# Kernel tuning notes

Hardware: AMD Instinct MI355X
Metric: run time of the kernel (lower is better)

Reference implementation:

```python
import jax, jax.numpy as jnp
import numpy as np
import math

B, S, D, H = 4, 1024, 1024, 16
DK = D // H
K_INDEX = 5


def setup_inputs() -> dict:
    key = jax.random.key(0)
    ks = jax.random.split(key, 10)
    s = 0.02
    return {
        "query": jax.random.normal(ks[0], (B, S, D), jnp.float32),
        "key": jax.random.normal(ks[1], (B, S, D), jnp.float32),
        "values": jax.random.normal(ks[2], (B, S, D), jnp.float32),
        "lens": jax.random.randint(ks[3], (B,), 0, S),
        "Wq": jax.random.normal(ks[4], (D, D), jnp.float32) * s,  # shared q/k proj (kq_same=True)
        "bq": jnp.zeros((D,), jnp.float32),
        "Wv": jax.random.normal(ks[5], (D, D), jnp.float32) * s,
        "bv": jnp.zeros((D,), jnp.float32),
        "Wo": jax.random.normal(ks[6], (D, D), jnp.float32) * s,
        "bo": jnp.zeros((D,), jnp.float32),
        "gammas": jax.random.normal(ks[7], (H, 1, 1), jnp.float32) * 0.1,
        "ln_w": jnp.ones((D,), jnp.float32),
        "ln_b": jnp.zeros((D,), jnp.float32),
    }


def _split_heads(x):
    b, s, _ = x.shape
    return x.reshape(b, s, H, DK).transpose(0, 2, 1, 3)  # [B,H,S,DK]


def reference(query, key, values, lens, Wq, bq, Wv, bv, Wo, bo, gammas, ln_w, ln_b):
    # causal mask, peek_cur=False -> strict lower triangle; eval mode (no random masking)
    mask = jnp.tril(jnp.ones((S, S), bool), -1)[None, None]  # [1,1,S,S]

    q = _split_heads(query @ Wq.T + bq)
    k = _split_heads(key @ Wq.T + bq)   # kq_same: shared weights
    v = _split_heads(values @ Wv.T + bv)

    scores = jnp.einsum("bhid,bhjd->bhij", q, k) / math.sqrt(DK)
    NEG = jnp.finfo(scores.dtype).min

    # --- distance-decay term (no_grad in torch -> stop_gradient) ---
    s_ = jax.nn.softmax(jnp.where(mask, scores, NEG), axis=-1)
    distcum = jnp.cumsum(s_, axis=-1)
    disttotal = jnp.sum(s_, axis=-1, keepdims=True)
    idx = jnp.arange(S, dtype=scores.dtype)
    pos_effect = jnp.abs(idx[None, :] - idx[:, None])[None, None]  # |j - i|
    dist = jnp.sqrt(jnp.clip((disttotal - distcum) * pos_effect, 0.0, None))
    dist = jax.lax.stop_gradient(dist)

    gam = -jnp.abs(gammas)[None]  # [1,H,1,1]
    total_effect = jnp.clip(jnp.exp(dist * gam), 1e-5, 1e5)
    scores = scores * total_effect

    scores = jnp.where(mask, scores, NEG)
    p = jax.nn.softmax(scores, axis=-1)
    p = jnp.where(mask, p, 0.0)

    # maxout rescale (peek_cur=False)
    scale = jnp.minimum(1.0 / jnp.max(p, axis=-1, keepdims=True), 5.0)
    p = p * scale

    attn = jnp.einsum("bhij,bhjd->bhid", p, v)
    concat = attn.transpose(0, 2, 1, 3).reshape(B, S, D)
    attn_out = concat @ Wo.T + bo

    # k_select sparsification of the (post-softmax, maxout-scaled) scores
    sc_a = p[:, :, :K_INDEX, :]
    sc_b = p[:, :, K_INDEX:, :]
    kth = jax.lax.top_k(sc_b, K_INDEX)[0][..., -1:]  # k-th largest per row
    sc_b = jnp.where(sc_b >= kth, sc_b, NEG)
    sparse_scores = jax.nn.softmax(jnp.concatenate([sc_a, sc_b], axis=2), axis=-1)

    # residual (eval: dropout is identity) + LayerNorm
    y = query + attn_out
    mu = jnp.mean(y, axis=-1, keepdims=True)
    var = jnp.mean((y - mu) ** 2, axis=-1, keepdims=True)
    out = (y - mu) / jnp.sqrt(var + 1e-5) * ln_w + ln_b
    return (out, sparse_scores)
```

## Files before the change

### kernel.cpp

```cpp
#include <hip/hip_runtime.h>
#include <hip/hip_fp16.h>

#define Ssz 1024
#define Dsz 1024
#define Hsz 16
#define DKsz 64
#define Bsz 4
#define NEGI (-1.0e30f)
#define NEGD (-1.0e300)

typedef float f32x4 __attribute__((ext_vector_type(4)));
typedef _Float16 f16x8 __attribute__((ext_vector_type(8)));
typedef _Float16 f16x4 __attribute__((ext_vector_type(4)));

__device__ __forceinline__ float wmaxf(float x) {
#pragma unroll
  for (int o = 32; o; o >>= 1) x = fmaxf(x, __shfl_xor(x, o));
  return x;
}
__device__ __forceinline__ float wsumf(float x) {
#pragma unroll
  for (int o = 32; o; o >>= 1) x += __shfl_xor(x, o);
  return x;
}
__device__ __forceinline__ double wmaxd(double x) {
#pragma unroll
  for (int o = 32; o; o >>= 1) x = fmax(x, __shfl_xor(x, o));
  return x;
}
__device__ __forceinline__ double wsumd(double x) {
#pragma unroll
  for (int o = 32; o; o >>= 1) x += __shfl_xor(x, o);
  return x;
}
__device__ __forceinline__ int wmini(int x) {
#pragma unroll
  for (int o = 32; o; o >>= 1) x = min(x, __shfl_xor(x, o));
  return x;
}
__device__ __forceinline__ int sswz(int c) { return c ^ (((c >> 5) & 7) << 2); }
__device__ __forceinline__ int pswz(int c, int r) { return c ^ (r & 7) ^ ((c >> 3) & 7); }

__global__ __launch_bounds__(256) void wsplit_qv(
    const float* __restrict__ Wq, const float* __restrict__ Wv,
    __half* __restrict__ wqhi, __half* __restrict__ wqlo, __half* __restrict__ wvhi) {
  const size_t i = ((size_t)blockIdx.x * 256 + threadIdx.x) * 4;
  const f32x4 q = *(const f32x4*)(Wq + i);
  const f32x4 v = *(const f32x4*)(Wv + i);
  f16x4 hq, lq, hv;
#pragma unroll
  for (int e = 0; e < 4; e++) {
    const _Float16 h = (_Float16)q[e];
    hq[e] = h;
    lq[e] = (_Float16)(q[e] - (float)h);
    hv[e] = (_Float16)v[e];
  }
  *(f16x4*)((_Float16*)wqhi + i) = hq;
  *(f16x4*)((_Float16*)wqlo + i) = lq;
  *(f16x4*)((_Float16*)wvhi + i) = hv;
}

__global__ __launch_bounds__(256) void wsplit_o(
    const float* __restrict__ Wo, __half* __restrict__ wohi) {
  const size_t i = ((size_t)blockIdx.x * 256 + threadIdx.x) * 4;
  const f32x4 v = *(const f32x4*)(Wo + i);
  f16x4 hv;
#pragma unroll
  for (int e = 0; e < 4; e++) hv[e] = (_Float16)v[e];
  *(f16x4*)((_Float16*)wohi + i) = hv;
}

__global__ __launch_bounds__(256) void gemm_qk(
    const float* __restrict__ A, const __half* __restrict__ wqhi,
    const __half* __restrict__ wqlo, const float* __restrict__ bias,
    __half* __restrict__ ohi, __half* __restrict__ olo) {
  const int w = threadIdx.x >> 6, lane = threadIdx.x & 63;
  const int quad = lane >> 4, l16 = lane & 15;
  const int m0 = blockIdx.x * 64 + w * 16;
  const int n0 = blockIdx.y * 64;
  f32x4 acc[4] = {};
  const size_t arow = (size_t)(m0 + l16) * Dsz;
  for (int k0 = 0; k0 < Dsz; k0 += 32) {
    f16x8 ahi, alo;
    {
      const float* ap = A + arow + k0 + quad * 8;
#pragma unroll
      for (int e = 0; e < 8; e++) {
        const float v = ap[e];
        const _Float16 h = (_Float16)v;
        ahi[e] = h;
        alo[e] = (_Float16)(v - (float)h);
      }
    }
#pragma unroll
    for (int t = 0; t < 4; t++) {
      const size_t woff = (size_t)(n0 + t * 16 + l16) * Dsz + k0 + quad * 8;
      const f16x8 whi = *(const f16x8*)((const _Float16*)wqhi + woff);
      const f16x8 wlo = *(const f16x8*)((const _Float16*)wqlo + woff);
      acc[t] = __builtin_amdgcn_mfma_f32_16x16x32_f16(ahi, whi, acc[t], 0, 0, 0);
      acc[t] = __builtin_amdgcn_mfma_f32_16x16x32_f16(ahi, wlo, acc[t], 0, 0, 0);
      acc[t] = __builtin_amdgcn_mfma_f32_16x16x32_f16(alo, whi, acc[t], 0, 0, 0);
    }
  }
#pragma unroll
  for (int t = 0; t < 4; t++) {
    const int oc = n0 + t * 16 + l16;
    const float bv = bias[oc];
    const int hh = oc >> 6, dk = oc & 63;
#pragma unroll
    for (int r = 0; r < 4; r++) {
      const int mr = m0 + quad * 4 + r;
      const int bb = mr >> 10, ss = mr & 1023;
      const float v = acc[t][r] + bv;
      const size_t idx = ((size_t)(bb * Hsz + hh) * Ssz + ss) * DKsz + dk;
      const __half h = __float2half(v);
      ohi[idx] = h;
      olo[idx] = __float2half(v - __half2float(h));
    }
  }
}

__global__ __launch_bounds__(256) void gemm_v(
    const float* __restrict__ A, const __half* __restrict__ wvhi,
    const float* __restrict__ bias, __half* __restrict__ out_t) {
  const int w = threadIdx.x >> 6, lane = threadIdx.x & 63;
  const int quad = lane >> 4, l16 = lane & 15;
  const int m0 = blockIdx.x * 64 + w * 16;
  const int n0 = blockIdx.y * 64;
  f32x4 acc[4] = {};
  const size_t arow = (size_t)(m0 + l16) * Dsz;
  for (int k0 = 0; k0 < Dsz; k0 += 32) {
    f16x8 ahi;
    {
      const float* ap = A + arow + k0 + quad * 8;
#pragma unroll
      for (int e = 0; e < 8; e++) ahi[e] = (_Float16)ap[e];
    }
#pragma unroll
    for (int t = 0; t < 4; t++) {
      const size_t woff = (size_t)(n0 + t * 16 + l16) * Dsz + k0 + quad * 8;
      const f16x8 whi = *(const f16x8*)((const _Float16*)wvhi + woff);
      acc[t] = __builtin_amdgcn_mfma_f32_16x16x32_f16(ahi, whi, acc[t], 0, 0, 0);
    }
  }
#pragma unroll
  for (int t = 0; t < 4; t++) {
    const int oc = n0 + t * 16 + l16;
    const float bv = bias[oc];
    const int hh = oc >> 6, dk = oc & 63;
#pragma unroll
    for (int r = 0; r < 4; r++) {
      const int mr = m0 + quad * 4 + r;
      const int bb = mr >> 10, ss = mr & 1023;
      out_t[((size_t)(bb * Hsz + hh) * DKsz + dk) * Ssz + ss] = __float2half(acc[t][r] + bv);
    }
  }
}

__global__ __launch_bounds__(256) void gemm_o(
    const __half* __restrict__ A, const __half* __restrict__ wohi,
    const float* __restrict__ bias, float* __restrict__ outf) {
  const int w = threadIdx.x >> 6, lane = threadIdx.x & 63;
  const int quad = lane >> 4, l16 = lane & 15;
  const int m0 = blockIdx.x * 64 + w * 16;
  const int n0 = blockIdx.y * 64;
  f32x4 acc[4] = {};
  const size_t arow = (size_t)(m0 + l16) * Dsz;
  for (int k0 = 0; k0 < Dsz; k0 += 32) {
    const f16x8 a = *(const f16x8*)(A + arow + k0 + quad * 8);
#pragma unroll
    for (int t = 0; t < 4; t++) {
      const size_t woff = (size_t)(n0 + t * 16 + l16) * Dsz + k0 + quad * 8;
      const f16x8 whi = *(const f16x8*)((const _Float16*)wohi + woff);
      acc[t] = __builtin_amdgcn_mfma_f32_16x16x32_f16(a, whi, acc[t], 0, 0, 0);
    }
  }
#pragma unroll
  for (int t = 0; t < 4; t++) {
    const int oc = n0 + t * 16 + l16;
    const float bv = bias[oc];
#pragma unroll
    for (int r = 0; r < 4; r++) {
      const int mr = m0 + quad * 4 + r;
      outf[(size_t)mr * Dsz + oc] = acc[t][r] + bv;
    }
  }
}


__global__ __launch_bounds__(256) void attn_scores(
    const __half* __restrict__ qhi, const __half* __restrict__ qlo,
    const __half* __restrict__ khi, const __half* __restrict__ klo,
    float* __restrict__ scores, int bh0) {
  const int w = threadIdx.x >> 6, lane = threadIdx.x & 63;
  const int quad = lane >> 4, l16 = lane & 15;
  const int lbh = blockIdx.y, bh = bh0 + lbh;
  for (int cc = 0; cc < 2; cc++) {
    const int chunk = cc ? (63 - (int)blockIdx.x) : (int)blockIdx.x;
    const int i0 = chunk * 16;
    const size_t qb = ((size_t)bh * Ssz + i0 + l16) * DKsz + quad * 8;
    const f16x8 ah0 = *(const f16x8*)(qhi + qb);
    const f16x8 ah1 = *(const f16x8*)(qhi + qb + 32);
    const f16x8 al0 = *(const f16x8*)(qlo + qb);
    const f16x8 al1 = *(const f16x8*)(qlo + qb + 32);
    float* dst = scores + ((size_t)lbh * Ssz + i0) * Ssz;
    for (int tt = 0; tt < 16; tt++) {
      const int n0 = (w + tt * 4) * 16;
      if (n0 > i0 + 14) continue;
      const size_t kb = ((size_t)bh * Ssz + n0 + l16) * DKsz + quad * 8;
      const f16x8 bh0v = *(const f16x8*)(khi + kb);
      const f16x8 bh1v = *(const f16x8*)(khi + kb + 32);
      const f16x8 bl0v = *(const f16x8*)(klo + kb);
      const f16x8 bl1v = *(const f16x8*)(klo + kb + 32);
      f32x4 accs = {};
      accs = __builtin_amdgcn_mfma_f32_16x16x32_f16(al0, bl0v, accs, 0, 0, 0);
      accs = __builtin_amdgcn_mfma_f32_16x16x32_f16(al1, bl1v, accs, 0, 0, 0);
      accs = __builtin_amdgcn_mfma_f32_16x16x32_f16(ah0, bl0v, accs, 0, 0, 0);
      accs = __builtin_amdgcn_mfma_f32_16x16x32_f16(ah1, bl1v, accs, 0, 0, 0);
      accs = __builtin_amdgcn_mfma_f32_16x16x32_f16(al0, bh0v, accs, 0, 0, 0);
      accs = __builtin_amdgcn_mfma_f32_16x16x32_f16(al1, bh1v, accs, 0, 0, 0);
      accs = __builtin_amdgcn_mfma_f32_16x16x32_f16(ah0, bh0v, accs, 0, 0, 0);
      accs = __builtin_amdgcn_mfma_f32_16x16x32_f16(ah1, bh1v, accs, 0, 0, 0);
#pragma unroll
      for (int r = 0; r < 4; r++)
        dst[(size_t)(quad * 4 + r) * Ssz + n0 + l16] = accs[r] * 0.125f;
    }
  }
}

__global__ __launch_bounds__(256) void attn_soft(
    float* __restrict__ scores, const float* __restrict__ gam,
    float* __restrict__ sparse, int bh0) {
  const int w = threadIdx.x >> 6, lane = threadIdx.x & 63;
  const int lbh = blockIdx.y, bh = bh0 + lbh;
  const int hidx = bh & 15;
  const float gf = -fabsf(gam[hidx]);
  for (int cc = 0; cc < 2; cc++) {
    const int chunk = cc ? (63 - (int)blockIdx.x) : (int)blockIdx.x;
    const int i0 = chunk * 16;
    for (int rr = 0; rr < 4; rr++) {
      const int gi = i0 + w * 4 + rr;
      const int nch = __builtin_amdgcn_readfirstlane((gi + 63) >> 6);
      float* rowp = scores + ((size_t)lbh * Ssz + gi) * Ssz;
      float xf[16];
      float m1 = NEGI;
#pragma unroll
      for (int e = 0; e < 16; e++) {
        if (e < nch) {
          const int j = 64 * e + lane;
          xf[e] = rowp[j];
          if (j < gi) m1 = fmaxf(m1, xf[e]);
        }
      }
      m1 = wmaxf(m1);
      float s[16];
      float ls = 0.f;
#pragma unroll
      for (int e = 0; e < 16; e++) {
        s[e] = 0.f;
        if (e < nch) {
          const int j = 64 * e + lane;
          const float v = (j < gi) ? __expf(xf[e] - m1) : 0.f;
          s[e] = v;
          ls += v;
        }
      }
      ls = wsumf(ls);
      const float invls = (ls > 0.f) ? 1.0f / ls : 0.f;
      float tot[16];
#pragma unroll
      for (int e = 0; e < 16; e++) {
        if (e < nch) {
          const float q = s[e] * invls;
          float v = __shfl_down(q, 1);
          if (lane == 63) v = 0.f;
#pragma unroll
          for (int o = 1; o < 64; o <<= 1) {
            const float t = __shfl_down(v, o);
            if (lane + o < 64) v += t;
          }
          s[e] = v;
          tot[e] = __shfl(q + v, 0);
        }
      }
      {
        float csum = 0.f;
#pragma unroll
        for (int e = 15; e >= 0; e--) {
          if (e < nch) {
            s[e] = s[e] + csum;
            csum += tot[e];
          }
        }
      }
      float ys[16];
      float m2 = NEGI;
#pragma unroll
      for (int e = 0; e < 16; e++) {
        ys[e] = NEGI;
        if (e < nch) {
          const int j = 64 * e + lane;
          if (j < gi) {
            const float pe = (float)(gi - j);
            const float tl = s[e] > 0.f ? s[e] * pe : 0.f;
            float te = __expf(gf * sqrtf(tl));
            te = te < 1e-5f ? 1e-5f : te;
            const float vv = xf[e] * te;
            ys[e] = vv;
            m2 = fmaxf(m2, vv);
          }
        }
      }
      m2 = wmaxf(m2);
      float xs[16];
      float ls3 = 0.f, mev = 0.f;
#pragma unroll
      for (int e = 0; e < 16; e++) {
        xs[e] = 0.f;
        if (e < nch) {
          const int j = 64 * e + lane;
          const float ev = (j < gi) ? __expf(ys[e] - m2) : 0.f;
          xs[e] = ev;
          ls3 += ev;
          mev = fmaxf(mev, ev);
        }
      }
      ls3 = wsumf(ls3);
      mev = wmaxf(mev);
      const float inv2 = (ls3 > 0.f) ? 1.0f / ls3 : 0.f;
      const float mp = mev * inv2;
      const float scl = (mp > 0.f) ? fminf(1.0f / mp, 5.0f) : 5.0f;
      const float c2 = inv2 * scl;
#pragma unroll
      for (int e = 0; e < 16; e++) xs[e] *= c2;
      const float m3 = mp * scl;
      {
        _Float16* prow = (_Float16*)rowp;
#pragma unroll
        for (int e = 0; e < 16; e++) prow[64 * e + lane] = (_Float16)xs[e];
      }

      float* dst = sparse + ((size_t)bh * Ssz + gi) * Ssz;
      if (gi < 5) {
        float o4[16];
        float ls4 = 0.f;
#pragma unroll
        for (int e = 0; e < 16; e++) {
          const float ev = expf(xs[e] - m3);
          o4[e] = ev;
          ls4 += ev;
        }
        const float inv3 = 1.0f / fmaxf(wsumf(ls4), 1e-30f);
#pragma unroll
        for (int e = 0; e < 16; e++) dst[64 * e + lane] = o4[e] * inv3;
      } else {
        float m5 = 0.f, m6 = 0.f;
        {
          unsigned int removed = 0;
          for (int r6 = 0; r6 < 6; r6++) {
            float lm = NEGI;
#pragma unroll
            for (int e = 0; e < 16; e++)
              if (!((removed >> e) & 1)) lm = fmaxf(lm, ys[e]);
            const float m = wmaxf(lm);
            const unsigned long long bal = __ballot(lm == m);
            const int src = __ffsll(bal) - 1;
            int rem_e = 0;
#pragma unroll
            for (int e = 15; e >= 0; e--)
              if (!((removed >> e) & 1) && ys[e] == m) rem_e = e;
            if (lane == src) removed |= 1u << rem_e;
            if (r6 == 4) m5 = m;
            if (r6 == 5) m6 = m;
          }
        }
        const float bstar = 0.5f * (m5 + m6);
        const float ETA = 6e-5f;
        const float wlo = m6 - 0.1f, whi = m5 + 0.1f;
        float md[16];
        float mn = 0.f;
#pragma unroll
        for (int e = 0; e < 16; e++) {
          md[e] = 0.f;
          if (e < nch) {
            const int j = 64 * e + lane;
            if (j < gi && ys[e] >= wlo && ys[e] <= whi) {
              const float pe = (float)(gi - j);
              const float t0 = fmaxf(s[e], 0.f);
              float telo = __expf(gf * sqrtf(fmaxf(t0 - ETA, 0.f) * pe));
              telo = fminf(fmaxf(telo, 1e-5f), 1.0f);
              float tehi = __expf(gf * sqrtf((t0 + ETA) * pe));
              tehi = fminf(fmaxf(tehi, 1e-5f), 1.0f);
              md[e] = fminf(fabsf(xf[e]) * (telo - tehi) + 2e-4f, 0.04f);
              mn = fmaxf(mn, md[e]);
            }
          }
        }
        mn = wmaxf(mn);
        float cnt = 0.f;
        unsigned int mK = 0, mA = 0;
#pragma unroll
        for (int e = 0; e < 16; e++) {
          if (e < nch) {
            const int j = 64 * e + lane;
            if (j < gi) {
              const float margin = fminf(1.5f * (md[e] + mn) + 1e-4f, 0.06f);
              if (ys[e] > bstar + margin) {
                mK |= 1u << e; cnt += 1.f;
              } else if (!(ys[e] < bstar - margin)) {
                mA |= 1u << e; cnt += 2048.f;
              }
            }
          }
        }
        cnt = wsumf(cnt);
        const float cA = floorf(cnt * (1.0f / 2048.0f));
        const float cK = cnt - 2048.0f * cA;
        float vvf[16];
        float vK = 0.f, vA = 0.f;
#pragma unroll
        for (int e = 0; e < 16; e++) {
          vvf[e] = 0.f;
          if (((mK | mA) >> e) & 1) {
            const float val = __expf(xs[e] - m3);
            vvf[e] = val;
            if ((mK >> e) & 1) vK += val; else vA += val;
          }
        }
        vK = wsumf(vK); vA = wsumf(vA);
        const float vbar = (cA > 0.5f) ? vA / cA : 0.f;
        const float Zhat = vK + (5.0f - cK) * vbar;
        const float invZ = (Zhat > 0.f) ? 1.0f / Zhat : 0.f;
#pragma unroll
        for (int e = 0; e < 16; e++) {
          const bool isK = (mK >> e) & 1;
          const bool isA = (mA >> e) & 1;
          const float o = isK ? vvf[e] * invZ : isA ? 0.5f * vvf[e] * invZ : 0.f;
          dst[64 * e + lane] = o;
        }
      }
    }
  }
}

__global__ __launch_bounds__(256) void attn_pv(
    const float* __restrict__ scoresP, const __half* __restrict__ vt,
    __half* __restrict__ attn_c, int bh0) {
  const int w = threadIdx.x >> 6, lane = threadIdx.x & 63;
  const int quad = lane >> 4, l16 = lane & 15;
  const int lbh = blockIdx.y, bh = bh0 + lbh;
  const int hidx = bh & 15, bidx = bh >> 4;
  const _Float16* pb = (const _Float16*)scoresP;
  const int dk0 = w * 16;
  for (int cc = 0; cc < 2; cc++) {
    const int chunk = cc ? (63 - (int)blockIdx.x) : (int)blockIdx.x;
    const int i0 = chunk * 16;
    const int kmax = (i0 + 15 + 31) & ~31;
    f32x4 acc = {};
    const size_t prow = ((size_t)lbh * Ssz + i0 + l16) * 2048;
    const size_t vrow = ((size_t)bh * DKsz + dk0 + l16) * Ssz;
    for (int k0 = 0; k0 < kmax; k0 += 32) {
      const f16x8 a = *(const f16x8*)(pb + prow + k0 + quad * 8);
      const f16x8 b = *(const f16x8*)(vt + vrow + k0 + quad * 8);
      acc = __builtin_amdgcn_mfma_f32_16x16x32_f16(a, b, acc, 0, 0, 0);
    }
#pragma unroll
    for (int r = 0; r < 4; r++) {
      const int ss = i0 + quad * 4 + r;
      attn_c[((size_t)bidx * Ssz + ss) * Dsz + hidx * DKsz + dk0 + l16] = __float2half(acc[r]);
    }
  }
}

__global__ __launch_bounds__(256) void attn_kernel(
    const __half* __restrict__ qhi, const __half* __restrict__ qlo,
    const __half* __restrict__ khi, const __half* __restrict__ klo,
    const __half* __restrict__ vt, const float* __restrict__ gam,
    __half* __restrict__ attn_c, float* __restrict__ sparse) {
  __shared__ __align__(16) float sc[16 * 1024];
  const int w = threadIdx.x >> 6, lane = threadIdx.x & 63;
  const int quad = lane >> 4, l16 = lane & 15;
  const int bh = blockIdx.y, i0 = blockIdx.x * 16;
  const int hidx = bh & 15, bidx = bh >> 4;
  _Float16* pbase = (_Float16*)sc;

  {
    const size_t qb = ((size_t)bh * Ssz + i0 + l16) * DKsz + quad * 8;
    const f16x8 ah0 = *(const f16x8*)(qhi + qb);
    const f16x8 ah1 = *(const f16x8*)(qhi + qb + 32);
    const f16x8 al0 = *(const f16x8*)(qlo + qb);
    const f16x8 al1 = *(const f16x8*)(qlo + qb + 32);
    for (int tt = 0; tt < 16; tt++) {
      const int n0 = (w + tt * 4) * 16;
      const size_t kb = ((size_t)bh * Ssz + n0 + l16) * DKsz + quad * 8;
      const f16x8 bh0 = *(const f16x8*)(khi + kb);
      const f16x8 bh1 = *(const f16x8*)(khi + kb + 32);
      const f16x8 bl0 = *(const f16x8*)(klo + kb);
      const f16x8 bl1 = *(const f16x8*)(klo + kb + 32);
      f32x4 accs = {};
      accs = __builtin_amdgcn_mfma_f32_16x16x32_f16(al0, bl0, accs, 0, 0, 0);
      accs = __builtin_amdgcn_mfma_f32_16x16x32_f16(al1, bl1, accs, 0, 0, 0);
      accs = __builtin_amdgcn_mfma_f32_16x16x32_f16(ah0, bl0, accs, 0, 0, 0);
      accs = __builtin_amdgcn_mfma_f32_16x16x32_f16(ah1, bl1, accs, 0, 0, 0);
      accs = __builtin_amdgcn_mfma_f32_16x16x32_f16(al0, bh0, accs, 0, 0, 0);
      accs = __builtin_amdgcn_mfma_f32_16x16x32_f16(al1, bh1, accs, 0, 0, 0);
      accs = __builtin_amdgcn_mfma_f32_16x16x32_f16(ah0, bh0, accs, 0, 0, 0);
      accs = __builtin_amdgcn_mfma_f32_16x16x32_f16(ah1, bh1, accs, 0, 0, 0);
      const int pc = sswz(n0 + l16);
#pragma unroll
      for (int r = 0; r < 4; r++)
        sc[(quad * 4 + r) * 1024 + pc] = accs[r] * 0.125f;
    }
  }
  __syncthreads();

  {
    const double g = -fabs((double)gam[hidx]);
    for (int rr = 0; rr < 4; rr++) {
      const int r = w * 4 + rr, gi = i0 + r;
      float xf[16];
#pragma unroll
      for (int q4 = 0; q4 < 4; q4++) {
        const f32x4 t = *(const f32x4*)(sc + r * 1024 + sswz(lane * 16 + q4 * 4));
#pragma unroll
        for (int e = 0; e < 4; e++) xf[q4 * 4 + e] = t[e];
      }
      float m1 = NEGI;
#pragma unroll
      for (int e = 0; e < 16; e++) {
        const int j = lane * 16 + e;
        if (j < gi) m1 = fmaxf(m1, xf[e]);
      }
      m1 = wmaxf(m1);
      double s[16];
      double ls = 0.0;
#pragma unroll
      for (int e = 0; e < 16; e++) {
        const int j = lane * 16 + e;
        const double v = (j < gi) ? exp((double)xf[e] - (double)m1) : 0.0;
        s[e] = v;
        ls += v;
      }
      ls = wsumd(ls);
      const double invls = (ls > 0.0) ? 1.0 / ls : 0.0;
      double lt = 0.0;
#pragma unroll
      for (int e = 0; e < 16; e++) { s[e] *= invls; lt += s[e]; }
      double v = __shfl_down(lt, 1);
      if (lane == 63) v = 0.0;
#pragma unroll
      for (int o = 1; o < 64; o <<= 1) {
        const double t = __shfl_down(v, o);
        if (lane + o < 64) v += t;
      }
      double run = v;
#pragma unroll
      for (int e = 15; e >= 0; e--) {
        const double tmp = s[e];
        s[e] = run;
        run += tmp;
      }
      double ys[16], xs[16];
      double m2 = NEGD;
#pragma unroll
      for (int e = 0; e < 16; e++) {
        const int j = lane * 16 + e;
        if (j < gi) {
          const double pe = (double)(gi - j);
          const double tl = s[e] > 0.0 ? s[e] * pe : 0.0;
          double te = exp(g * sqrt(tl));
          te = te < 1e-5 ? 1e-5 : te;
          const double vv = (double)xf[e] * te;
          ys[e] = vv;
          m2 = fmax(m2, vv);
        } else {
          ys[e] = NEGD;
        }
      }
      m2 = wmaxd(m2);
      double ls3 = 0.0;
#pragma unroll
      for (int e = 0; e < 16; e++) {
        const int j = lane * 16 + e;
        const double ev = (j < gi) ? exp(ys[e] - m2) : 0.0;
        xs[e] = ev;
        ls3 += ev;
      }
      ls3 = wsumd(ls3);
      const double inv2 = (ls3 > 0.0) ? 1.0 / ls3 : 0.0;
      double mp = 0.0;
#pragma unroll
      for (int e = 0; e < 16; e++) {
        xs[e] *= inv2;
        mp = fmax(mp, xs[e]);
      }
      mp = wmaxd(mp);
      const double scl = (mp > 0.0) ? fmin(1.0 / mp, 5.0) : 5.0;
#pragma unroll
      for (int e = 0; e < 16; e++) xs[e] *= scl;
      {
        __align__(16) _Float16 hb[16];
#pragma unroll
        for (int e = 0; e < 16; e++) hb[e] = (_Float16)(float)xs[e];
        const int c0 = lane * 2;
        *(f16x8*)(pbase + r * 2048 + pswz(c0, r) * 8) = *(const f16x8*)&hb[0];
        *(f16x8*)(pbase + r * 2048 + pswz(c0 + 1, r) * 8) = *(const f16x8*)&hb[8];
      }
      double m3 = 0.0;
#pragma unroll
      for (int e = 0; e < 16; e++) m3 = fmax(m3, xs[e]);
      m3 = wmaxd(m3);

      float* dst = sparse + ((size_t)bh * Ssz + gi) * Ssz + lane * 16;
      if (gi < 5) {
        float o4[16];
        float ls4 = 0.f;
#pragma unroll
        for (int e = 0; e < 16; e++) {
          const float ev = expf((float)(xs[e] - m3));
          o4[e] = ev;
          ls4 += ev;
        }
        const float inv3 = 1.0f / fmaxf(wsumf(ls4), 1e-30f);
#pragma unroll
        for (int q4 = 0; q4 < 4; q4++) {
          f32x4 st;
#pragma unroll
          for (int e = 0; e < 4; e++) st[e] = o4[q4 * 4 + e] * inv3;
          *(f32x4*)(dst + q4 * 4) = st;
        }
      } else {
        double m5 = 0.0, m6 = 0.0;
        {
          unsigned int removed = 0;
          for (int r6 = 0; r6 < 6; r6++) {
            double lm = NEGD;
#pragma unroll
            for (int e = 0; e < 16; e++)
              if (!((removed >> e) & 1)) lm = fmax(lm, ys[e]);
            const double m = wmaxd(lm);
            int li = 1 << 30;
#pragma unroll
            for (int e = 0; e < 16; e++)
              if (!((removed >> e) & 1) && ys[e] == m) li = min(li, lane * 16 + e);
            li = wmini(li);
            if ((li >> 4) == lane) removed |= 1u << (li & 15);
            if (r6 == 4) m5 = m;
            if (r6 == 5) m6 = m;
          }
        }
        const double bstar = 0.5 * (m5 + m6);
        const double ETA = 6e-5;
        double md[16];
#pragma unroll
        for (int e = 0; e < 16; e++) {
          const int j = lane * 16 + e;
          if (j < gi) {
            const double pe = (double)(gi - j);
            const double t0 = fmax(s[e], 0.0);
            double telo = exp(g * sqrt(fmax(t0 - ETA, 0.0) * pe));
            telo = fmin(fmax(telo, 1e-5), 1.0);
            double tehi = exp(g * sqrt((t0 + ETA) * pe));
            tehi = fmin(fmax(tehi, 1e-5), 1.0);
            md[e] = fmin(fabs((double)xf[e]) * (telo - tehi) + 2e-4, 0.04);
          } else {
            md[e] = 0.0;
          }
        }
        double mn = 0.0;
#pragma unroll
        for (int e = 0; e < 16; e++) {
          const int j = lane * 16 + e;
          if (j < gi && ys[e] >= m6 - 0.1 && ys[e] <= m5 + 0.1) mn = fmax(mn, md[e]);
        }
        mn = wmaxd(mn);
        double vK = 0.0, vA = 0.0, cK = 0.0, cA = 0.0;
        double vv[16];
        int cls[16];
#pragma unroll
        for (int e = 0; e < 16; e++) {
          const int j = lane * 16 + e;
          if (j < gi) {
            const double margin = fmin(1.5 * (md[e] + mn) + 1e-4, 0.06);
            const double val = exp(xs[e] - m3);
            vv[e] = val;
            if (ys[e] > bstar + margin) {
              cls[e] = 2; vK += val; cK += 1.0;
            } else if (ys[e] < bstar - margin) {
              cls[e] = 0;
            } else {
              cls[e] = 1; vA += val; cA += 1.0;
            }
          } else {
            cls[e] = 0;
            vv[e] = 0.0;
          }
        }
        vK = wsumd(vK); vA = wsumd(vA);
        cK = wsumd(cK); cA = wsumd(cA);
        const double vbar = (cA > 0.5) ? vA / cA : 0.0;
        const double Zhat = vK + (5.0 - cK) * vbar;
        const double invZ = (Zhat > 0.0) ? 1.0 / Zhat : 0.0;
#pragma unroll
        for (int q4 = 0; q4 < 4; q4++) {
          f32x4 st;
#pragma unroll
          for (int e4 = 0; e4 < 4; e4++) {
            const int e = q4 * 4 + e4;
            const double o =
                (cls[e] == 2) ? vv[e] * invZ : (cls[e] == 1) ? 0.5 * vv[e] * invZ : 0.0;
            st[e4] = (float)o;
          }
          *(f32x4*)(dst + q4 * 4) = st;
        }
      }
    }
  }
  __syncthreads();

  {
    const int dk0 = w * 16;
    f32x4 acc = {};
    for (int k0 = 0; k0 < Ssz; k0 += 32) {
      const int cch = (k0 >> 3) + quad;
      const f16x8 a = *(const f16x8*)(pbase + l16 * 2048 + pswz(cch, l16) * 8);
      const f16x8 b =
          *(const f16x8*)(vt + ((size_t)bh * DKsz + dk0 + l16) * Ssz + k0 + quad * 8);
      acc = __builtin_amdgcn_mfma_f32_16x16x32_f16(a, b, acc, 0, 0, 0);
    }
#pragma unroll
    for (int r = 0; r < 4; r++) {
      const int ss = i0 + quad * 4 + r;
      attn_c[((size_t)bidx * Ssz + ss) * Dsz + hidx * DKsz + dk0 + l16] = __float2half(acc[r]);
    }
  }
}

__global__ __launch_bounds__(256) void ln_kernel(
    const float* __restrict__ query, const float* __restrict__ attn_out,
    const float* __restrict__ ln_w, const float* __restrict__ ln_b,
    float* __restrict__ out) {
  __shared__ float red[8];
  const int n = blockIdx.x, t = threadIdx.x;
  const int w = t >> 6, lane = t & 63;
  float y[4];
  float s = 0.f, s2 = 0.f;
#pragma unroll
  for (int k = 0; k < 4; k++) {
    const int j = t + k * 256;
    const float v = query[(size_t)n * Dsz + j] + attn_out[(size_t)n * Dsz + j];
    y[k] = v;
    s += v;
    s2 += v * v;
  }
  s = wsumf(s);
  s2 = wsumf(s2);
  if (lane == 0) { red[w] = s; red[4 + w] = s2; }
  __syncthreads();
  s = red[0] + red[1] + red[2] + red[3];
  s2 = red[4] + red[5] + red[6] + red[7];
  const float mu = s * (1.0f / 1024.0f);
  const float var = fmaxf(s2 * (1.0f / 1024.0f) - mu * mu, 0.0f);
  const float rs = rsqrtf(var + 1e-5f);
#pragma unroll
  for (int k = 0; k < 4; k++) {
    const int j = t + k * 256;
    out[(size_t)n * Dsz + j] = (y[k] - mu) * rs * ln_w[j] + ln_b[j];
  }
}

extern "C" void kernel_launch(void* const* d_in, const int* in_sizes, int n_in,
                              void* d_out, int out_size, void* d_ws, size_t ws_size,
                              hipStream_t stream) {
  (void)in_sizes; (void)n_in; (void)out_size;
  const float* query = (const float*)d_in[0];
  const float* key = (const float*)d_in[1];
  const float* values = (const float*)d_in[2];
  const float* Wq = (const float*)d_in[4];
  const float* bq = (const float*)d_in[5];
  const float* Wv = (const float*)d_in[6];
  const float* bv = (const float*)d_in[7];
  const float* Wo = (const float*)d_in[8];
  const float* bo = (const float*)d_in[9];
  const float* gam = (const float*)d_in[10];
  const float* lnw = (const float*)d_in[11];
  const float* lnb = (const float*)d_in[12];

  char* ws = (char*)d_ws;
  const size_t MB = 1024u * 1024u;
  const size_t MB8 = 8u * MB;
  __half* qhi = (__half*)ws;
  __half* qlo = (__half*)(ws + 1 * MB8);
  __half* khi = (__half*)(ws + 2 * MB8);
  __half* klo = (__half*)(ws + 3 * MB8);
  __half* vt = (__half*)(ws + 4 * MB8);
  __half* attn_c = (__half*)(ws + 5 * MB8);
  float* attn_out = (float*)ws;
  float* scores = (float*)(ws + 6 * MB8);

  __half* wqhi = (__half*)(ws + 5 * MB8);
  __half* wqlo = (__half*)(ws + 5 * MB8 + 2 * MB);
  __half* wvhi = (__half*)(ws + 5 * MB8 + 4 * MB);
  __half* wohi = (__half*)(ws + 2 * MB8);

  float* out = (float*)d_out;
  float* sparse = out + (size_t)Bsz * Ssz * Dsz;

  const size_t avail = (ws_size > 6 * MB8) ? (ws_size - 6 * MB8) : 0;
  int cbh = 0;
  if (avail >= 64u * 4u * MB) cbh = 64;
  else if (avail >= 32u * 4u * MB) cbh = 32;
  else if (avail >= 16u * 4u * MB) cbh = 16;
  else if (avail >= 8u * 4u * MB) cbh = 8;

  const dim3 gg(64, 16), gb(256);
  wsplit_qv<<<1024, 256, 0, stream>>>(Wq, Wv, wqhi, wqlo, wvhi);
  gemm_qk<<<gg, gb, 0, stream>>>(query, wqhi, wqlo, bq, qhi, qlo);
  gemm_qk<<<gg, gb, 0, stream>>>(key, wqhi, wqlo, bq, khi, klo);
  gemm_v<<<gg, gb, 0, stream>>>(values, wvhi, bv, vt);
  if (cbh > 0) {
    for (int bh0 = 0; bh0 < Bsz * Hsz; bh0 += cbh) {
      attn_scores<<<dim3(32, cbh), 256, 0, stream>>>(qhi, qlo, khi, klo, scores, bh0);
      attn_soft<<<dim3(32, cbh), 256, 0, stream>>>(scores, gam, sparse, bh0);
      attn_pv<<<dim3(32, cbh), 256, 0, stream>>>(scores, vt, attn_c, bh0);
    }
  } else {
    attn_kernel<<<dim3(64, 64), 256, 0, stream>>>(qhi, qlo, khi, klo, vt, gam, attn_c, sparse);
  }
  wsplit_o<<<1024, 256, 0, stream>>>(Wo, wohi);
  gemm_o<<<gg, gb, 0, stream>>>(attn_c, wohi, bo, attn_out);
  ln_kernel<<<(Bsz * Ssz), 256, 0, stream>>>(query, attn_out, lnw, lnb, out);
}
```

Measured before the change: 1.334 ms.

## Pre-split activations to fp16 and vectorize softmax rows with paired-column lanes

Adds separate kernels that convert the query, key and value activations into fp16 hi/lo buffers, staged in the output's sparse region, before the projection GEMMs. The GEMMs then load vectorized halves instead of converting fp32 scalars inside the k-loop. The attention softmax kernel now gives each lane two adjacent columns, so loads and stores become 8-byte vectors and half as many wave prefix scans are needed; the cumsum normalization is applied afterwards. The cost is extra kernel launches and extra global traffic for the split buffers, plus reuse of the output area as scratch.

```diff
diff --git a/kernel.cpp b/kernel.cpp
--- a/kernel.cpp
+++ b/kernel.cpp
@@ -10,8 +10,10 @@
 #define NEGD (-1.0e300)
 
 typedef float f32x4 __attribute__((ext_vector_type(4)));
+typedef float f32x2 __attribute__((ext_vector_type(2)));
 typedef _Float16 f16x8 __attribute__((ext_vector_type(8)));
 typedef _Float16 f16x4 __attribute__((ext_vector_type(4)));
+typedef _Float16 f16x2 __attribute__((ext_vector_type(2)));
 
 __device__ __forceinline__ float wmaxf(float x) {
 #pragma unroll
@@ -70,10 +72,35 @@
   *(f16x4*)((_Float16*)wohi + i) = hv;
 }
 
+__global__ __launch_bounds__(256) void asplit_hl(
+    const float* __restrict__ A, __half* __restrict__ hi, __half* __restrict__ lo) {
+  const size_t i = ((size_t)blockIdx.x * 256 + threadIdx.x) * 4;
+  const f32x4 v = *(const f32x4*)(A + i);
+  f16x4 h, l;
+#pragma unroll
+  for (int e = 0; e < 4; e++) {
+    const _Float16 hh = (_Float16)v[e];
+    h[e] = hh;
+    l[e] = (_Float16)(v[e] - (float)hh);
+  }
+  *(f16x4*)((_Float16*)hi + i) = h;
+  *(f16x4*)((_Float16*)lo + i) = l;
+}
+
+__global__ __launch_bounds__(256) void asplit_h(
+    const float* __restrict__ A, __half* __restrict__ hi) {
+  const size_t i = ((size_t)blockIdx.x * 256 + threadIdx.x) * 4;
+  const f32x4 v = *(const f32x4*)(A + i);
+  f16x4 h;
+#pragma unroll
+  for (int e = 0; e < 4; e++) h[e] = (_Float16)v[e];
+  *(f16x4*)((_Float16*)hi + i) = h;
+}
+
 __global__ __launch_bounds__(256) void gemm_qk(
-    const float* __restrict__ A, const __half* __restrict__ wqhi,
-    const __half* __restrict__ wqlo, const float* __restrict__ bias,
-    __half* __restrict__ ohi, __half* __restrict__ olo) {
+    const __half* __restrict__ Ahi, const __half* __restrict__ Alo,
+    const __half* __restrict__ wqhi, const __half* __restrict__ wqlo,
+    const float* __restrict__ bias, __half* __restrict__ ohi, __half* __restrict__ olo) {
   const int w = threadIdx.x >> 6, lane = threadIdx.x & 63;
   const int quad = lane >> 4, l16 = lane & 15;
   const int m0 = blockIdx.x * 64 + w * 16;
@@ -81,17 +108,8 @@
   f32x4 acc[4] = {};
   const size_t arow = (size_t)(m0 + l16) * Dsz;
   for (int k0 = 0; k0 < Dsz; k0 += 32) {
-    f16x8 ahi, alo;
-    {
-      const float* ap = A + arow + k0 + quad * 8;
-#pragma unroll
-      for (int e = 0; e < 8; e++) {
-        const float v = ap[e];
-        const _Float16 h = (_Float16)v;
-        ahi[e] = h;
-        alo[e] = (_Float16)(v - (float)h);
-      }
-    }
+    const f16x8 ahi = *(const f16x8*)((const _Float16*)Ahi + arow + k0 + quad * 8);
+    const f16x8 alo = *(const f16x8*)((const _Float16*)Alo + arow + k0 + quad * 8);
 #pragma unroll
     for (int t = 0; t < 4; t++) {
       const size_t woff = (size_t)(n0 + t * 16 + l16) * Dsz + k0 + quad * 8;
@@ -121,7 +139,7 @@
 }
 
 __global__ __launch_bounds__(256) void gemm_v(
-    const float* __restrict__ A, const __half* __restrict__ wvhi,
+    const __half* __restrict__ Ahi, const __half* __restrict__ wvhi,
     const float* __restrict__ bias, __half* __restrict__ out_t) {
   const int w = threadIdx.x >> 6, lane = threadIdx.x & 63;
   const int quad = lane >> 4, l16 = lane & 15;
@@ -130,12 +148,7 @@
   f32x4 acc[4] = {};
   const size_t arow = (size_t)(m0 + l16) * Dsz;
   for (int k0 = 0; k0 < Dsz; k0 += 32) {
-    f16x8 ahi;
-    {
-      const float* ap = A + arow + k0 + quad * 8;
-#pragma unroll
-      for (int e = 0; e < 8; e++) ahi[e] = (_Float16)ap[e];
-    }
+    const f16x8 ahi = *(const f16x8*)((const _Float16*)Ahi + arow + k0 + quad * 8);
 #pragma unroll
     for (int t = 0; t < 4; t++) {
       const size_t woff = (size_t)(n0 + t * 16 + l16) * Dsz + k0 + quad * 8;
@@ -235,94 +248,110 @@
   const int lbh = blockIdx.y, bh = bh0 + lbh;
   const int hidx = bh & 15;
   const float gf = -fabsf(gam[hidx]);
+  const int jb = 2 * lane;
   for (int cc = 0; cc < 2; cc++) {
     const int chunk = cc ? (63 - (int)blockIdx.x) : (int)blockIdx.x;
     const int i0 = chunk * 16;
     for (int rr = 0; rr < 4; rr++) {
       const int gi = i0 + w * 4 + rr;
-      const int nch = __builtin_amdgcn_readfirstlane((gi + 63) >> 6);
+      const int nch = __builtin_amdgcn_readfirstlane((gi + 127) >> 7);
       float* rowp = scores + ((size_t)lbh * Ssz + gi) * Ssz;
       float xf[16];
       float m1 = NEGI;
 #pragma unroll
-      for (int e = 0; e < 16; e++) {
+      for (int e = 0; e < 8; e++) {
         if (e < nch) {
-          const int j = 64 * e + lane;
-          xf[e] = rowp[j];
-          if (j < gi) m1 = fmaxf(m1, xf[e]);
+          const int j0 = 128 * e + jb;
+          const f32x2 t = *(const f32x2*)(rowp + j0);
+          xf[2 * e] = t[0];
+          xf[2 * e + 1] = t[1];
+          if (j0 < gi) m1 = fmaxf(m1, t[0]);
+          if (j0 + 1 < gi) m1 = fmaxf(m1, t[1]);
         }
       }
       m1 = wmaxf(m1);
       float s[16];
-      float ls = 0.f;
-#pragma unroll
-      for (int e = 0; e < 16; e++) {
-        s[e] = 0.f;
+#pragma unroll
+      for (int k = 0; k < 16; k++) s[k] = 0.f;
+#pragma unroll
+      for (int e = 0; e < 8; e++) {
         if (e < nch) {
-          const int j = 64 * e + lane;
-          const float v = (j < gi) ? __expf(xf[e] - m1) : 0.f;
-          s[e] = v;
-          ls += v;
-        }
-      }
-      ls = wsumf(ls);
-      const float invls = (ls > 0.f) ? 1.0f / ls : 0.f;
-      float tot[16];
-#pragma unroll
-      for (int e = 0; e < 16; e++) {
+          const int j0 = 128 * e + jb;
+          if (j0 < gi) s[2 * e] = __expf(xf[2 * e] - m1);
+          if (j0 + 1 < gi) s[2 * e + 1] = __expf(xf[2 * e + 1] - m1);
+        }
+      }
+      float tot[8];
+#pragma unroll
+      for (int e = 0; e < 8; e++) {
         if (e < nch) {
-          const float q = s[e] * invls;
-          float v = __shfl_down(q, 1);
+          const float q2 = s[2 * e] + s[2 * e + 1];
+          float v = __shfl_down(q2, 1);
           if (lane == 63) v = 0.f;
 #pragma unroll
           for (int o = 1; o < 64; o <<= 1) {
             const float t = __shfl_down(v, o);
             if (lane + o < 64) v += t;
           }
-          s[e] = v;
-          tot[e] = __shfl(q + v, 0);
-        }
-      }
-      {
-        float csum = 0.f;
-#pragma unroll
-        for (int e = 15; e >= 0; e--) {
-          if (e < nch) {
-            s[e] = s[e] + csum;
-            csum += tot[e];
-          }
-        }
-      }
+          tot[e] = __shfl(q2 + v, 0);
+          const float t1 = v;
+          const float t0e = v + s[2 * e + 1];
+          s[2 * e] = t0e;
+          s[2 * e + 1] = t1;
+        }
+      }
+      float csum = 0.f;
+#pragma unroll
+      for (int e = 7; e >= 0; e--) {
+        if (e < nch) {
+          s[2 * e] += csum;
+          s[2 * e + 1] += csum;
+          csum += tot[e];
+        }
+      }
+      const float ls = csum;
+      const float invls = (ls > 0.f) ? 1.0f / ls : 0.f;
       float ys[16];
       float m2 = NEGI;
 #pragma unroll
-      for (int e = 0; e < 16; e++) {
-        ys[e] = NEGI;
+      for (int k = 0; k < 16; k++) ys[k] = NEGI;
+#pragma unroll
+      for (int e = 0; e < 8; e++) {
         if (e < nch) {
-          const int j = 64 * e + lane;
-          if (j < gi) {
-            const float pe = (float)(gi - j);
-            const float tl = s[e] > 0.f ? s[e] * pe : 0.f;
-            float te = __expf(gf * sqrtf(tl));
-            te = te < 1e-5f ? 1e-5f : te;
-            const float vv = xf[e] * te;
-            ys[e] = vv;
-            m2 = fmaxf(m2, vv);
+#pragma unroll
+          for (int i = 0; i < 2; i++) {
+            const int j = 128 * e + jb + i;
+            if (j < gi) {
+              const float pe = (float)(gi - j);
+              const float tn = s[2 * e + i] * invls;
+              const float tl = tn > 0.f ? tn * pe : 0.f;
+              float te = __expf(gf * sqrtf(tl));
+              te = te < 1e-5f ? 1e-5f : te;
+              const float vv = xf[2 * e + i] * te;
+              ys[2 * e + i] = vv;
+              m2 = fmaxf(m2, vv);
+            }
           }
         }
       }
       m2 = wmaxf(m2);
       float xs[16];
+#pragma unroll
+      for (int k = 0; k < 16; k++) xs[k] = 0.f;
       float ls3 = 0.f, mev = 0.f;
 #pragma unroll
-      for (int e = 0; e < 16; e++) {
-        xs[e] = 0.f;
+      for (int e = 0; e < 8; e++) {
         if (e < nch) {
-          const int j = 64 * e + lane;
-          const float ev = (j < gi) ? __expf(ys[e] - m2) : 0.f;
-          xs[e] = ev;
-          ls3 += ev;
-          mev = fmaxf(mev, ev);
+#pragma unroll
+          for (int i = 0; i < 2; i++) {
+            const int j = 128 * e + jb + i;
+            if (j < gi) {
+              const float ev = __expf(ys[2 * e + i] - m2);
+              xs[2 * e + i] = ev;
+              ls3 += ev;
+              mev = fmaxf(mev, ev);
+            }
+          }
         }
       }
       ls3 = wsumf(ls3);
@@ -332,12 +361,17 @@
       const float scl = (mp > 0.f) ? fminf(1.0f / mp, 5.0f) : 5.0f;
       const float c2 = inv2 * scl;
 #pragma unroll
-      for (int e = 0; e < 16; e++) xs[e] *= c2;
+      for (int k = 0; k < 16; k++) xs[k] *= c2;
       const float m3 = mp * scl;
       {
         _Float16* prow = (_Float16*)rowp;
 #pragma unroll
-        for (int e = 0; e < 16; e++) prow[64 * e + lane] = (_Float16)xs[e];
+        for (int e = 0; e < 8; e++) {
+          f16x2 hp;
+          hp[0] = (_Float16)xs[2 * e];
+          hp[1] = (_Float16)xs[2 * e + 1];
+          *(f16x2*)(prow + 128 * e + jb) = hp;
+        }
       }
 
       float* dst = sparse + ((size_t)bh * Ssz + gi) * Ssz;
@@ -345,14 +379,19 @@
         float o4[16];
         float ls4 = 0.f;
 #pragma unroll
-        for (int e = 0; e < 16; e++) {
-          const float ev = expf(xs[e] - m3);
-          o4[e] = ev;
+        for (int k = 0; k < 16; k++) {
+          const float ev = expf(xs[k] - m3);
+          o4[k] = ev;
           ls4 += ev;
         }
         const float inv3 = 1.0f / fmaxf(wsumf(ls4), 1e-30f);
 #pragma unroll
-        for (int e = 0; e < 16; e++) dst[64 * e + lane] = o4[e] * inv3;
+        for (int e = 0; e < 8; e++) {
+          f32x2 st;
+          st[0] = o4[2 * e] * inv3;
+          st[1] = o4[2 * e + 1] * inv3;
+          *(f32x2*)(dst + 128 * e + jb) = st;
+        }
       } else {
         float m5 = 0.f, m6 = 0.f;
         {
@@ -360,16 +399,16 @@
           for (int r6 = 0; r6 < 6; r6++) {
             float lm = NEGI;
 #pragma unroll
-            for (int e = 0; e < 16; e++)
-              if (!((removed >> e) & 1)) lm = fmaxf(lm, ys[e]);
+            for (int k = 0; k < 16; k++)
+              if (!((removed >> k) & 1)) lm = fmaxf(lm, ys[k]);
             const float m = wmaxf(lm);
             const unsigned long long bal = __ballot(lm == m);
             const int src = __ffsll(bal) - 1;
-            int rem_e = 0;
-#pragma unroll
-            for (int e = 15; e >= 0; e--)
-              if (!((removed >> e) & 1) && ys[e] == m) rem_e = e;
-            if (lane == src) removed |= 1u << rem_e;
+            int rem_k = 0;
+#pragma unroll
+            for (int k = 15; k >= 0; k--)
+              if (!((removed >> k) & 1) && ys[k] == m) rem_k = k;
+            if (lane == src) removed |= 1u << rem_k;
             if (r6 == 4) m5 = m;
             if (r6 == 5) m6 = m;
           }
@@ -380,19 +419,24 @@
         float md[16];
         float mn = 0.f;
 #pragma unroll
-        for (int e = 0; e < 16; e++) {
-          md[e] = 0.f;
+        for (int e = 0; e < 8; e++) {
+          md[2 * e] = 0.f;
+          md[2 * e + 1] = 0.f;
           if (e < nch) {
-            const int j = 64 * e + lane;
-            if (j < gi && ys[e] >= wlo && ys[e] <= whi) {
-              const float pe = (float)(gi - j);
-              const float t0 = fmaxf(s[e], 0.f);
-              float telo = __expf(gf * sqrtf(fmaxf(t0 - ETA, 0.f) * pe));
-              telo = fminf(fmaxf(telo, 1e-5f), 1.0f);
-              float tehi = __expf(gf * sqrtf((t0 + ETA) * pe));
-              tehi = fminf(fmaxf(tehi, 1e-5f), 1.0f);
-              md[e] = fminf(fabsf(xf[e]) * (telo - tehi) + 2e-4f, 0.04f);
-              mn = fmaxf(mn, md[e]);
+#pragma unroll
+            for (int i = 0; i < 2; i++) {
+              const int j = 128 * e + jb + i;
+              const int k = 2 * e + i;
+              if (j < gi && ys[k] >= wlo && ys[k] <= whi) {
+                const float pe = (float)(gi - j);
+                const float t0 = fmaxf(s[k] * invls, 0.f);
+                float telo = __expf(gf * sqrtf(fmaxf(t0 - ETA, 0.f) * pe));
+                telo = fminf(fmaxf(telo, 1e-5f), 1.0f);
+                float tehi = __expf(gf * sqrtf((t0 + ETA) * pe));
+                tehi = fminf(fmaxf(tehi, 1e-5f), 1.0f);
+                md[k] = fminf(fabsf(xf[k]) * (telo - tehi) + 2e-4f, 0.04f);
+                mn = fmaxf(mn, md[k]);
+              }
             }
           }
         }
@@ -400,15 +444,19 @@
         float cnt = 0.f;
         unsigned int mK = 0, mA = 0;
 #pragma unroll
-        for (int e = 0; e < 16; e++) {
+        for (int e = 0; e < 8; e++) {
           if (e < nch) {
-            const int j = 64 * e + lane;
-            if (j < gi) {
-              const float margin = fminf(1.5f * (md[e] + mn) + 1e-4f, 0.06f);
-              if (ys[e] > bstar + margin) {
-                mK |= 1u << e; cnt += 1.f;
-              } else if (!(ys[e] < bstar - margin)) {
-                mA |= 1u << e; cnt += 2048.f;
+#pragma unroll
+            for (int i = 0; i < 2; i++) {
+              const int j = 128 * e + jb + i;
+              const int k = 2 * e + i;
+              if (j < gi) {
+                const float margin = fminf(1.5f * (md[k] + mn) + 1e-4f, 0.06f);
+                if (ys[k] > bstar + margin) {
+                  mK |= 1u << k; cnt += 1.f;
+                } else if (!(ys[k] < bstar - margin)) {
+                  mA |= 1u << k; cnt += 2048.f;
+                }
               }
             }
           }
@@ -419,12 +467,12 @@
         float vvf[16];
         float vK = 0.f, vA = 0.f;
 #pragma unroll
-        for (int e = 0; e < 16; e++) {
-          vvf[e] = 0.f;
-          if (((mK | mA) >> e) & 1) {
-            const float val = __expf(xs[e] - m3);
-            vvf[e] = val;
-            if ((mK >> e) & 1) vK += val; else vA += val;
+        for (int k = 0; k < 16; k++) {
+          vvf[k] = 0.f;
+          if (((mK | mA) >> k) & 1) {
+            const float val = __expf(xs[k] - m3);
+            vvf[k] = val;
+            if ((mK >> k) & 1) vK += val; else vA += val;
           }
         }
         vK = wsumf(vK); vA = wsumf(vA);
@@ -432,11 +480,16 @@
         const float Zhat = vK + (5.0f - cK) * vbar;
         const float invZ = (Zhat > 0.f) ? 1.0f / Zhat : 0.f;
 #pragma unroll
-        for (int e = 0; e < 16; e++) {
-          const bool isK = (mK >> e) & 1;
-          const bool isA = (mA >> e) & 1;
-          const float o = isK ? vvf[e] * invZ : isA ? 0.5f * vvf[e] * invZ : 0.f;
-          dst[64 * e + lane] = o;
+        for (int e = 0; e < 8; e++) {
+          f32x2 st;
+#pragma unroll
+          for (int i = 0; i < 2; i++) {
+            const int k = 2 * e + i;
+            const bool isK = (mK >> k) & 1;
+            const bool isA = (mA >> k) & 1;
+            st[i] = isK ? vvf[k] * invZ : isA ? 0.5f * vvf[k] * invZ : 0.f;
+          }
+          *(f32x2*)(dst + 128 * e + jb) = st;
         }
       }
     }
@@ -806,6 +859,10 @@
   float* out = (float*)d_out;
   float* sparse = out + (size_t)Bsz * Ssz * Dsz;
 
+  __half* sa_hi = (__half*)((char*)sparse);
+  __half* sa_lo = (__half*)((char*)sparse + 8 * MB);
+  __half* sv = (__half*)((char*)sparse + 16 * MB);
+
   const size_t avail = (ws_size > 6 * MB8) ? (ws_size - 6 * MB8) : 0;
   int cbh = 0;
   if (avail >= 64u * 4u * MB) cbh = 64;
@@ -815,9 +872,12 @@
 
   const dim3 gg(64, 16), gb(256);
   wsplit_qv<<<1024, 256, 0, stream>>>(Wq, Wv, wqhi, wqlo, wvhi);
-  gemm_qk<<<gg, gb, 0, stream>>>(query, wqhi, wqlo, bq, qhi, qlo);
-  gemm_qk<<<gg, gb, 0, stream>>>(key, wqhi, wqlo, bq, khi, klo);
-  gemm_v<<<gg, gb, 0, stream>>>(values, wvhi, bv, vt);
+  asplit_hl<<<4096, 256, 0, stream>>>(query, sa_hi, sa_lo);
+  gemm_qk<<<gg, gb, 0, stream>>>(sa_hi, sa_lo, wqhi, wqlo, bq, qhi, qlo);
+  asplit_hl<<<4096, 256, 0, stream>>>(key, sa_hi, sa_lo);
+  gemm_qk<<<gg, gb, 0, stream>>>(sa_hi, sa_lo, wqhi, wqlo, bq, khi, klo);
+  asplit_h<<<4096, 256, 0, stream>>>(values, sv);
+  gemm_v<<<gg, gb, 0, stream>>>(sv, wvhi, bv, vt);
   if (cbh > 0) {
     for (int bh0 = 0; bh0 < Bsz * Hsz; bh0 += cbh) {
       attn_scores<<<dim3(32, cbh), 256, 0, stream>>>(qhi, qlo, khi, klo, scores, bh0);
```

Result: faster. 1.274 ms (-4.5%).
